# Optimization experiments

Hardware: AMD Instinct MI355X
Metric: run time of the kernel (lower is better)

Reference implementation:

```python
import jax, jax.numpy as jnp
import numpy as np

B, N = 8, 2048
IN_F, MID1, HID, MID2, OUT_F = 128, 128, 128, 128, 128
BIG = 9e15  # matches torch's 9000000000000000.0 additive mask constant


def _linear_params(key, out_d, in_d):
    # torch Linear layout: W is [out, in]
    kw, kb = jax.random.split(key)
    w = jax.random.normal(kw, (out_d, in_d), jnp.float32) * (1.0 / np.sqrt(in_d))
    b = jax.random.normal(kb, (out_d,), jnp.float32) * 0.01
    return w, b


def setup_inputs() -> dict:
    key = jax.random.key(0)
    ks = jax.random.split(key, 16)
    h = jax.random.normal(ks[0], (B, N, IN_F), jnp.float32)
    adj = jax.random.randint(ks[1], (B, N, N), 0, 2).astype(jnp.float32)
    vae2_fetures = jax.random.normal(ks[2], (B, N, OUT_F), jnp.float32)
    Wv1, bv1 = _linear_params(ks[3], MID1, IN_F)
    Wk1, bk1 = _linear_params(ks[4], MID1, IN_F)
    Wq1, bq1 = _linear_params(ks[5], MID1, IN_F)
    Wo1, bo1 = _linear_params(ks[6], HID, MID1)
    Wv2, bv2 = _linear_params(ks[7], MID2, HID)
    Wk2, bk2 = _linear_params(ks[8], MID2, HID)
    Wq2, bq2 = _linear_params(ks[9], MID2, HID)
    Wo2, bo2 = _linear_params(ks[10], OUT_F, MID2)
    Wf, bf = _linear_params(ks[11], OUT_F, 2 * OUT_F)
    return {
        "h": h, "adj": adj, "vae2_fetures": vae2_fetures,
        "Wv1": Wv1, "bv1": bv1, "Wk1": Wk1, "bk1": bk1, "Wq1": Wq1, "bq1": bq1,
        "Wo1": Wo1, "bo1": bo1,
        "Wv2": Wv2, "bv2": bv2, "Wk2": Wk2, "bk2": bk2, "Wq2": Wq2, "bq2": bq2,
        "Wo2": Wo2, "bo2": bo2, "Wf": Wf, "bf": bf,
    }


def _lin(x, W, b):
    return jnp.einsum('bnd,od->bno', x, W) + b


def _masked_att_block(x, adj, Wq, bq, Wk, bk, Wv, bv):
    v = jax.nn.relu(_lin(x, Wv, bv))          # [B,N,D]
    q = jax.nn.relu(_lin(x, Wq, bq))          # [B,N,D]
    k = jax.nn.relu(_lin(x, Wk, bk))          # [B,N,D]
    s = jnp.einsum('bnd,bmd->bnm', q, k)       # [B,N,N]
    masked = s * adj - BIG * (1.0 - adj)       # multiplicative + additive mask
    att = jax.nn.softmax(masked, axis=-1)
    return jnp.einsum('bnm,bmd->bnd', att, v)


def reference(h, adj, vae2_fetures,
              Wv1, bv1, Wk1, bk1, Wq1, bq1, Wo1, bo1,
              Wv2, bv2, Wk2, bk2, Wq2, bq2, Wo2, bo2,
              Wf, bf):
    f1 = _masked_att_block(h, adj, Wq1, bq1, Wk1, bk1, Wv1, bv1)
    f1 = _lin(f1, Wo1, bo1)                    # [B,N,HID]
    f2 = _masked_att_block(f1, adj, Wq2, bq2, Wk2, bk2, Wv2, bv2)
    f2 = _lin(f2, Wo2, bo2)                    # [B,N,OUT_F]
    f3 = jnp.concatenate([f2, vae2_fetures], axis=2)
    return _lin(f3, Wf, bf)                    # [B,N,OUT_F]
```

## Files before the change

### kernel.cpp

```cpp
#include <hip/hip_runtime.h>

typedef short s16x8 __attribute__((ext_vector_type(8)));
typedef float f32x4 __attribute__((ext_vector_type(4)));
typedef unsigned short u16x4v __attribute__((ext_vector_type(4)));

#define NEGF (-1e30f)
#define NSPLIT 4
#define NROWS 16384

__device__ __forceinline__ float bf2f(unsigned short u) {
  union { unsigned int i; float f; } v; v.i = ((unsigned int)u) << 16; return v.f;
}
__device__ __forceinline__ unsigned short f2bf(float f) {
  union { float fl; unsigned int i; } v; v.fl = f;
  unsigned int x = v.i;
  x += 0x7fffu + ((x >> 16) & 1u);
  return (unsigned short)(x >> 16);
}
__device__ __forceinline__ s16x8 load8_bf16(const unsigned short* p) {
  return *(const s16x8*)p;
}
__device__ __forceinline__ s16x8 load8_f32(const float* p) {
  float4 a = *(const float4*)p;
  float4 b = *(const float4*)(p + 4);
  s16x8 r;
  r[0] = (short)f2bf(a.x); r[1] = (short)f2bf(a.y);
  r[2] = (short)f2bf(a.z); r[3] = (short)f2bf(a.w);
  r[4] = (short)f2bf(b.x); r[5] = (short)f2bf(b.y);
  r[6] = (short)f2bf(b.z); r[7] = (short)f2bf(b.w);
  return r;
}

#define OW_Q1 0
#define OW_K1 16384
#define OW_V1 32768
#define OW_O1 49152
#define OW_Q2 65536
#define OW_K2 81920
#define OW_V2 98304
#define OW_O2 114688
#define OW_F  131072
#define OB_Q1 163840
#define OB_K1 163968
#define OB_V1 164096
#define OB_O1 164224
#define OB_Q2 164352
#define OB_K2 164480
#define OB_V2 164608
#define OB_O2 164736
#define OB_F  164864

__global__ __launch_bounds__(256) void conv_w_kernel(
    const float* s0, const float* s1, const float* s2, const float* s3,
    const float* s4, const float* s5, const float* s6, const float* s7,
    const float* s8, const float* s9, const float* s10, const float* s11,
    const float* s12, const float* s13, const float* s14, const float* s15,
    const float* s16, const float* s17, unsigned short* dst)
{
  const float* src; int count; int off;
  switch (blockIdx.y) {
    case 0:  src = s0;  count = 16384; off = OW_Q1; break;
    case 1:  src = s1;  count = 16384; off = OW_K1; break;
    case 2:  src = s2;  count = 16384; off = OW_V1; break;
    case 3:  src = s3;  count = 16384; off = OW_O1; break;
    case 4:  src = s4;  count = 16384; off = OW_Q2; break;
    case 5:  src = s5;  count = 16384; off = OW_K2; break;
    case 6:  src = s6;  count = 16384; off = OW_V2; break;
    case 7:  src = s7;  count = 16384; off = OW_O2; break;
    case 8:  src = s8;  count = 32768; off = OW_F;  break;
    case 9:  src = s9;  count = 128;   off = OB_Q1; break;
    case 10: src = s10; count = 128;   off = OB_K1; break;
    case 11: src = s11; count = 128;   off = OB_V1; break;
    case 12: src = s12; count = 128;   off = OB_O1; break;
    case 13: src = s13; count = 128;   off = OB_Q2; break;
    case 14: src = s14; count = 128;   off = OB_K2; break;
    case 15: src = s15; count = 128;   off = OB_V2; break;
    case 16: src = s16; count = 128;   off = OB_O2; break;
    default: src = s17; count = 128;   off = OB_F;  break;
  }
  for (int i = blockIdx.x * 256 + threadIdx.x; i < count; i += gridDim.x * 256)
    dst[off + i] = f2bf(src[i]);
}

__global__ __launch_bounds__(256) void pack_adj_kernel(
    const float* __restrict__ adj, unsigned long long* __restrict__ mask)
{
  const size_t stride = (size_t)gridDim.x * 256;
  const size_t total = (size_t)NROWS * 2048;
  for (size_t i = (size_t)blockIdx.x * 256 + threadIdx.x; i < total; i += stride) {
    unsigned long long m = __ballot(adj[i] != 0.0f);
    if ((threadIdx.x & 63) == 0) mask[i >> 6] = m;
  }
}

template <bool A1F32, int MODE>
__device__ __forceinline__ void gemm_body(
    const void* __restrict__ A1, const unsigned short* __restrict__ W1,
    const unsigned short* __restrict__ bias, unsigned short* __restrict__ out)
{
  const int t = threadIdx.x;
  const int w = t >> 6;
  const int lane = t & 63;
  const int l15 = lane & 15;
  const int quad = lane >> 4;
  const int mbase = blockIdx.x * 16;

  s16x8 a1[4];
  if (A1F32) {
    const float* ar = (const float*)A1 + (size_t)(mbase + l15) * 128;
#pragma unroll
    for (int ks = 0; ks < 4; ++ks) a1[ks] = load8_f32(ar + ks * 32 + quad * 8);
  } else {
    const unsigned short* ar = (const unsigned short*)A1 + (size_t)(mbase + l15) * 128;
#pragma unroll
    for (int ks = 0; ks < 4; ++ks) a1[ks] = load8_bf16(ar + ks * 32 + quad * 8);
  }

#pragma unroll
  for (int nt = 0; nt < 2; ++nt) {
    const int n = (w * 2 + nt) * 16 + l15;
    f32x4 acc = {0.f, 0.f, 0.f, 0.f};
    const unsigned short* wr = W1 + (size_t)n * 128;
#pragma unroll
    for (int ks = 0; ks < 4; ++ks)
      acc = __builtin_amdgcn_mfma_f32_16x16x32_bf16(
          a1[ks], load8_bf16(wr + ks * 32 + quad * 8), acc, 0, 0, 0);
    const float bv = bf2f(bias[n]);
    if (MODE == 0) {
#pragma unroll
      for (int r = 0; r < 4; ++r) {
        float v = fmaxf(acc[r] + bv, 0.f);
        out[(size_t)(mbase + quad * 4 + r) * 128 + n] = f2bf(v);
      }
    } else {
      const int b  = mbase >> 11;
      const int nn = (mbase & 2047) + quad * 4;
      u16x4v pk;
#pragma unroll
      for (int r = 0; r < 4; ++r) pk[r] = f2bf(fmaxf(acc[r] + bv, 0.f));
      *(u16x4v*)(out + (size_t)(b * 128 + n) * 2048 + nn) = pk;
    }
  }
}

template <bool A1F32>
__global__ __launch_bounds__(256) void qkv_kernel(
    const void* __restrict__ x,
    const unsigned short* __restrict__ Wq, const unsigned short* __restrict__ bq, unsigned short* __restrict__ oq,
    const unsigned short* __restrict__ Wk, const unsigned short* __restrict__ bk, unsigned short* __restrict__ ok,
    const unsigned short* __restrict__ Wv, const unsigned short* __restrict__ bv, unsigned short* __restrict__ ovt)
{
  if (blockIdx.y == 0)      gemm_body<A1F32, 0>(x, Wq, bq, oq);
  else if (blockIdx.y == 1) gemm_body<A1F32, 0>(x, Wk, bk, ok);
  else                      gemm_body<A1F32, 1>(x, Wv, bv, ovt);
}

__global__ __launch_bounds__(256, 2) void attn_kernel(
    const unsigned short* __restrict__ Q,
    const unsigned short* __restrict__ K,
    const unsigned short* __restrict__ VT,
    const unsigned long long* __restrict__ MASK,
    float* __restrict__ pO, float* __restrict__ pm, float* __restrict__ pl)
{
  __shared__ __align__(16) unsigned short kbuf[64][136];
  __shared__ __align__(16) unsigned short vbuf[128][72];
  __shared__ __align__(16) unsigned short pbuf[4][32][72];

  const int t = threadIdx.x;
  const int w = t >> 6;
  const int lane = t & 63;
  const int l15 = lane & 15;
  const int quad = lane >> 4;

  const int gq0 = blockIdx.x * 128;
  const int b   = gq0 >> 11;
  const int q0  = gq0 & 2047;
  const int wq0 = q0 + w * 32;
  const int kc0 = blockIdx.y * 512;
  const int kc1 = kc0 + 512;

  const unsigned short* Kb  = K  + (size_t)(b * 2048) * 128;
  const unsigned short* VTb = VT + (size_t)(b * 128) * 2048;
  const unsigned long long* Mb = MASK + (size_t)b * 2048 * 32;

  s16x8 qf[2][4];
#pragma unroll
  for (int mt = 0; mt < 2; ++mt) {
    const unsigned short* qrow = Q + (size_t)(gq0 + w * 32 + mt * 16 + l15) * 128;
#pragma unroll
    for (int ks = 0; ks < 4; ++ks) qf[mt][ks] = load8_bf16(qrow + ks * 32 + quad * 8);
  }

  float mstate[2][4], lstate[2][4];
  f32x4 accO[2][8];
#pragma unroll
  for (int mt = 0; mt < 2; ++mt) {
#pragma unroll
    for (int r = 0; r < 4; ++r) { mstate[mt][r] = NEGF; lstate[mt][r] = 0.f; }
#pragma unroll
    for (int dt = 0; dt < 8; ++dt) accO[mt][dt] = (f32x4){0.f, 0.f, 0.f, 0.f};
  }

  s16x8 kr[4], vr[4];
#pragma unroll
  for (int i = 0; i < 4; ++i) {
    int slot = i * 256 + t;
    kr[i] = load8_bf16(Kb + (size_t)(kc0 + (slot >> 4)) * 128 + (slot & 15) * 8);
    vr[i] = load8_bf16(VTb + (size_t)(slot >> 3) * 2048 + kc0 + (slot & 7) * 8);
  }

  for (int kc = kc0; kc < kc1; kc += 64) {
    __syncthreads();
#pragma unroll
    for (int i = 0; i < 4; ++i) {
      int slot = i * 256 + t;
      *(s16x8*)&kbuf[slot >> 4][(slot & 15) * 8] = kr[i];
      *(s16x8*)&vbuf[slot >> 3][(slot & 7) * 8]  = vr[i];
    }
    __syncthreads();
    if (kc + 64 < kc1) {
#pragma unroll
      for (int i = 0; i < 4; ++i) {
        int slot = i * 256 + t;
        kr[i] = load8_bf16(Kb + (size_t)(kc + 64 + (slot >> 4)) * 128 + (slot & 15) * 8);
        vr[i] = load8_bf16(VTb + (size_t)(slot >> 3) * 2048 + (kc + 64) + (slot & 7) * 8);
      }
    }

    f32x4 sv[2][4];
#pragma unroll
    for (int nt = 0; nt < 4; ++nt) {
      sv[0][nt] = (f32x4){0.f, 0.f, 0.f, 0.f};
      sv[1][nt] = (f32x4){0.f, 0.f, 0.f, 0.f};
#pragma unroll
      for (int ks = 0; ks < 4; ++ks) {
        s16x8 kf = *(const s16x8*)&kbuf[nt * 16 + l15][ks * 32 + quad * 8];
        sv[0][nt] = __builtin_amdgcn_mfma_f32_16x16x32_bf16(qf[0][ks], kf, sv[0][nt], 0, 0, 0);
        sv[1][nt] = __builtin_amdgcn_mfma_f32_16x16x32_bf16(qf[1][ks], kf, sv[1][nt], 0, 0, 0);
      }
    }

    float chmax[2][4];
#pragma unroll
    for (int mt = 0; mt < 2; ++mt) {
#pragma unroll
      for (int r = 0; r < 4; ++r) {
        unsigned long long mw = Mb[(size_t)(wq0 + mt * 16 + quad * 4 + r) * 32 + (kc >> 6)];
        float cm = NEGF;
#pragma unroll
        for (int nt = 0; nt < 4; ++nt) {
          float s = ((mw >> (nt * 16 + l15)) & 1ull) ? sv[mt][nt][r] : NEGF;
          sv[mt][nt][r] = s;
          cm = fmaxf(cm, s);
        }
        chmax[mt][r] = cm;
      }
    }
#pragma unroll
    for (int d = 1; d < 16; d <<= 1) {
#pragma unroll
      for (int mt = 0; mt < 2; ++mt)
#pragma unroll
        for (int r = 0; r < 4; ++r)
          chmax[mt][r] = fmaxf(chmax[mt][r], __shfl_xor(chmax[mt][r], d, 64));
    }

    float mnew[2][4], alpha[2][4], rsum[2][4];
#pragma unroll
    for (int mt = 0; mt < 2; ++mt)
#pragma unroll
      for (int r = 0; r < 4; ++r) {
        mnew[mt][r] = fmaxf(mstate[mt][r], chmax[mt][r]);
        alpha[mt][r] = __expf(mstate[mt][r] - mnew[mt][r]);
        rsum[mt][r] = 0.f;
      }
#pragma unroll
    for (int mt = 0; mt < 2; ++mt)
#pragma unroll
      for (int nt = 0; nt < 4; ++nt)
#pragma unroll
        for (int r = 0; r < 4; ++r) {
          float p = __expf(sv[mt][nt][r] - mnew[mt][r]);
          rsum[mt][r] += p;
          pbuf[w][mt * 16 + quad * 4 + r][nt * 16 + l15] = f2bf(p);
        }
#pragma unroll
    for (int d = 1; d < 16; d <<= 1) {
#pragma unroll
      for (int mt = 0; mt < 2; ++mt)
#pragma unroll
        for (int r = 0; r < 4; ++r)
          rsum[mt][r] += __shfl_xor(rsum[mt][r], d, 64);
    }
#pragma unroll
    for (int mt = 0; mt < 2; ++mt)
#pragma unroll
      for (int r = 0; r < 4; ++r) {
        lstate[mt][r] = lstate[mt][r] * alpha[mt][r] + rsum[mt][r];
        mstate[mt][r] = mnew[mt][r];
      }
#pragma unroll
    for (int mt = 0; mt < 2; ++mt)
#pragma unroll
      for (int dt = 0; dt < 8; ++dt)
#pragma unroll
        for (int r = 0; r < 4; ++r) accO[mt][dt][r] *= alpha[mt][r];

    s16x8 pf[2][2];
#pragma unroll
    for (int mt = 0; mt < 2; ++mt)
#pragma unroll
      for (int ks = 0; ks < 2; ++ks)
        pf[mt][ks] = *(const s16x8*)&pbuf[w][mt * 16 + l15][ks * 32 + quad * 8];
#pragma unroll
    for (int dt = 0; dt < 8; ++dt) {
#pragma unroll
      for (int ks = 0; ks < 2; ++ks) {
        s16x8 vf = *(const s16x8*)&vbuf[dt * 16 + l15][ks * 32 + quad * 8];
        accO[0][dt] = __builtin_amdgcn_mfma_f32_16x16x32_bf16(pf[0][ks], vf, accO[0][dt], 0, 0, 0);
        accO[1][dt] = __builtin_amdgcn_mfma_f32_16x16x32_bf16(pf[1][ks], vf, accO[1][dt], 0, 0, 0);
      }
    }
  }

  float* pOs = pO + (size_t)blockIdx.y * NROWS * 128;
#pragma unroll
  for (int mt = 0; mt < 2; ++mt)
#pragma unroll
    for (int dt = 0; dt < 8; ++dt) {
      int dcol = dt * 16 + l15;
#pragma unroll
      for (int r = 0; r < 4; ++r) {
        int qg = gq0 + w * 32 + mt * 16 + quad * 4 + r;
        pOs[(size_t)qg * 128 + dcol] = accO[mt][dt][r];
      }
    }
  if (l15 == 0) {
#pragma unroll
    for (int mt = 0; mt < 2; ++mt)
#pragma unroll
      for (int r = 0; r < 4; ++r) {
        int qg = gq0 + w * 32 + mt * 16 + quad * 4 + r;
        pm[blockIdx.y * NROWS + qg] = mstate[mt][r];
        pl[blockIdx.y * NROWS + qg] = lstate[mt][r];
      }
  }
}

template <bool FINAL>
__global__ __launch_bounds__(256) void red_lin_kernel(
    const float* __restrict__ pO, const float* __restrict__ pm,
    const float* __restrict__ pl,
    const unsigned short* __restrict__ Wo, const unsigned short* __restrict__ bo,
    const unsigned short* __restrict__ Wf, const float* __restrict__ vae2,
    const unsigned short* __restrict__ bfb,
    unsigned short* __restrict__ out_bf, float* __restrict__ out_f32)
{
  __shared__ __align__(16) unsigned short At[16][136];
  __shared__ __align__(16) unsigned short Bt[16][136];

  const int t = threadIdx.x;
  const int grow0 = blockIdx.x * 16;

  {
    const int row = t >> 4;
    const int col8 = (t & 15) * 8;
    const int grow = grow0 + row;
    float ms[NSPLIT], mstar = NEGF;
#pragma unroll
    for (int s = 0; s < NSPLIT; ++s) {
      ms[s] = pm[s * NROWS + grow];
      mstar = fmaxf(mstar, ms[s]);
    }
    float wgt[NSPLIT], lstar = 0.f;
#pragma unroll
    for (int s = 0; s < NSPLIT; ++s) {
      wgt[s] = __expf(ms[s] - mstar);
      lstar += wgt[s] * pl[s * NROWS + grow];
    }
    const float inv = (lstar > 0.f) ? 1.f / lstar : 0.f;
    float acc8[8];
#pragma unroll
    for (int i = 0; i < 8; ++i) acc8[i] = 0.f;
#pragma unroll
    for (int s = 0; s < NSPLIT; ++s) {
      const float* p = pO + (size_t)s * NROWS * 128 + (size_t)grow * 128 + col8;
      float4 x0 = *(const float4*)p;
      float4 x1 = *(const float4*)(p + 4);
      acc8[0] += wgt[s] * x0.x; acc8[1] += wgt[s] * x0.y;
      acc8[2] += wgt[s] * x0.z; acc8[3] += wgt[s] * x0.w;
      acc8[4] += wgt[s] * x1.x; acc8[5] += wgt[s] * x1.y;
      acc8[6] += wgt[s] * x1.z; acc8[7] += wgt[s] * x1.w;
    }
#pragma unroll
    for (int i = 0; i < 8; ++i) At[row][col8 + i] = f2bf(acc8[i] * inv);
  }
  __syncthreads();

  const int w = t >> 6;
  const int lane = t & 63;
  const int l15 = lane & 15;
  const int quad = lane >> 4;

  s16x8 a[4];
#pragma unroll
  for (int ks = 0; ks < 4; ++ks) a[ks] = *(const s16x8*)&At[l15][ks * 32 + quad * 8];
#pragma unroll
  for (int nt = 0; nt < 2; ++nt) {
    const int n = (w * 2 + nt) * 16 + l15;
    f32x4 acc = {0.f, 0.f, 0.f, 0.f};
    const unsigned short* wr = Wo + (size_t)n * 128;
#pragma unroll
    for (int ks = 0; ks < 4; ++ks)
      acc = __builtin_amdgcn_mfma_f32_16x16x32_bf16(
          a[ks], load8_bf16(wr + ks * 32 + quad * 8), acc, 0, 0, 0);
    const float bv = bf2f(bo[n]);
    if (!FINAL) {
#pragma unroll
      for (int r = 0; r < 4; ++r)
        out_bf[(size_t)(grow0 + quad * 4 + r) * 128 + n] = f2bf(acc[r] + bv);
    } else {
#pragma unroll
      for (int r = 0; r < 4; ++r)
        Bt[quad * 4 + r][n] = f2bf(acc[r] + bv);
    }
  }

  if (FINAL) {
    __syncthreads();
    s16x8 a1[4], a2[4];
#pragma unroll
    for (int ks = 0; ks < 4; ++ks) a1[ks] = *(const s16x8*)&Bt[l15][ks * 32 + quad * 8];
    const float* vrow = vae2 + (size_t)(grow0 + l15) * 128;
#pragma unroll
    for (int ks = 0; ks < 4; ++ks) a2[ks] = load8_f32(vrow + ks * 32 + quad * 8);
#pragma unroll
    for (int nt = 0; nt < 2; ++nt) {
      const int n = (w * 2 + nt) * 16 + l15;
      f32x4 acc = {0.f, 0.f, 0.f, 0.f};
      const unsigned short* wr = Wf + (size_t)n * 256;
#pragma unroll
      for (int ks = 0; ks < 4; ++ks)
        acc = __builtin_amdgcn_mfma_f32_16x16x32_bf16(
            a1[ks], load8_bf16(wr + ks * 32 + quad * 8), acc, 0, 0, 0);
#pragma unroll
      for (int ks = 0; ks < 4; ++ks)
        acc = __builtin_amdgcn_mfma_f32_16x16x32_bf16(
            a2[ks], load8_bf16(wr + 128 + ks * 32 + quad * 8), acc, 0, 0, 0);
      const float bv = bf2f(bfb[n]);
#pragma unroll
      for (int r = 0; r < 4; ++r)
        out_f32[(size_t)(grow0 + quad * 4 + r) * 128 + n] = acc[r] + bv;
    }
  }
}

extern "C" void kernel_launch(void* const* d_in, const int* in_sizes, int n_in,
                              void* d_out, int out_size, void* d_ws, size_t ws_size,
                              hipStream_t stream)
{
  const float* h    = (const float*)d_in[0];
  const float* adj  = (const float*)d_in[1];
  const float* vae2 = (const float*)d_in[2];
  const float* Wv1  = (const float*)d_in[3];
  const float* bv1  = (const float*)d_in[4];
  const float* Wk1  = (const float*)d_in[5];
  const float* bk1  = (const float*)d_in[6];
  const float* Wq1  = (const float*)d_in[7];
  const float* bq1  = (const float*)d_in[8];
  const float* Wo1  = (const float*)d_in[9];
  const float* bo1  = (const float*)d_in[10];
  const float* Wv2  = (const float*)d_in[11];
  const float* bv2  = (const float*)d_in[12];
  const float* Wk2  = (const float*)d_in[13];
  const float* bk2  = (const float*)d_in[14];
  const float* Wq2  = (const float*)d_in[15];
  const float* bq2  = (const float*)d_in[16];
  const float* Wo2  = (const float*)d_in[17];
  const float* bo2  = (const float*)d_in[18];
  const float* Wf   = (const float*)d_in[19];
  const float* bff  = (const float*)d_in[20];

  char* wsb = (char*)d_ws;
  const size_t MB = 1u << 20;
  unsigned short* s_q  = (unsigned short*)(wsb + 0 * MB);
  unsigned short* s_k  = (unsigned short*)(wsb + 4 * MB);
  unsigned short* s_vt = (unsigned short*)(wsb + 8 * MB);
  unsigned short* s_f  = (unsigned short*)(wsb + 12 * MB);
  unsigned short* wbf  = (unsigned short*)(wsb + 16 * MB);
  unsigned long long* maskp = (unsigned long long*)(wsb + 17 * MB);
  float* pO = (float*)(wsb + 21 * MB);
  float* pm = (float*)(wsb + 53 * MB);
  float* pl = (float*)(wsb + 53 * MB + 512 * 1024);

  dim3 blk(256);
  conv_w_kernel<<<dim3(128, 18), blk, 0, stream>>>(
      Wq1, Wk1, Wv1, Wo1, Wq2, Wk2, Wv2, Wo2, Wf,
      bq1, bk1, bv1, bo1, bq2, bk2, bv2, bo2, bff, wbf);
  pack_adj_kernel<<<dim3(8192), blk, 0, stream>>>(adj, maskp);

  qkv_kernel<true><<<dim3(1024, 3), blk, 0, stream>>>(
      h, wbf + OW_Q1, wbf + OB_Q1, s_q,
         wbf + OW_K1, wbf + OB_K1, s_k,
         wbf + OW_V1, wbf + OB_V1, s_vt);
  attn_kernel<<<dim3(128, NSPLIT), blk, 0, stream>>>(s_q, s_k, s_vt, maskp, pO, pm, pl);
  red_lin_kernel<false><<<dim3(1024), blk, 0, stream>>>(
      pO, pm, pl, wbf + OW_O1, wbf + OB_O1, nullptr, nullptr, nullptr, s_f, nullptr);

  qkv_kernel<false><<<dim3(1024, 3), blk, 0, stream>>>(
      s_f, wbf + OW_Q2, wbf + OB_Q2, s_q,
           wbf + OW_K2, wbf + OB_K2, s_k,
           wbf + OW_V2, wbf + OB_V2, s_vt);
  attn_kernel<<<dim3(128, NSPLIT), blk, 0, stream>>>(s_q, s_k, s_vt, maskp, pO, pm, pl);
  red_lin_kernel<true><<<dim3(1024), blk, 0, stream>>>(
      pO, pm, pl, wbf + OW_O2, wbf + OB_O2, wbf + OW_F, vae2, wbf + OB_F,
      nullptr, (float*)d_out);
}
```

Before: 429.0 us.

## Fuse reduce with next QKV, drop weight conversion, reshape attention without LDS staging

The standalone weight-conversion kernel is removed, and the GEMMs now read fp32 weights directly, converting them to bf16 on the fly. The split-combine plus output-projection kernel is fused with the second layer's QKV projection, which removes one launch and the round trip of the intermediate features. The attention kernel moves to 128-thread blocks over 64 query rows and reads K and V fragments straight from global memory instead of double-buffering them in LDS. The adjacency packer now uses float4 loads and shuffle-OR reductions. The risks are more redundant global and L2 traffic for K/V and weights, and repeated fp32-to-bf16 conversion in every block.

```diff
diff --git a/kernel.cpp b/kernel.cpp
--- a/kernel.cpp
+++ b/kernel.cpp
@@ -8,9 +8,6 @@
 #define NSPLIT 4
 #define NROWS 16384
 
-__device__ __forceinline__ float bf2f(unsigned short u) {
-  union { unsigned int i; float f; } v; v.i = ((unsigned int)u) << 16; return v.f;
-}
 __device__ __forceinline__ unsigned short f2bf(float f) {
   union { float fl; unsigned int i; } v; v.fl = f;
   unsigned int x = v.i;
@@ -31,72 +28,29 @@
   return r;
 }
 
-#define OW_Q1 0
-#define OW_K1 16384
-#define OW_V1 32768
-#define OW_O1 49152
-#define OW_Q2 65536
-#define OW_K2 81920
-#define OW_V2 98304
-#define OW_O2 114688
-#define OW_F  131072
-#define OB_Q1 163840
-#define OB_K1 163968
-#define OB_V1 164096
-#define OB_O1 164224
-#define OB_Q2 164352
-#define OB_K2 164480
-#define OB_V2 164608
-#define OB_O2 164736
-#define OB_F  164864
-
-__global__ __launch_bounds__(256) void conv_w_kernel(
-    const float* s0, const float* s1, const float* s2, const float* s3,
-    const float* s4, const float* s5, const float* s6, const float* s7,
-    const float* s8, const float* s9, const float* s10, const float* s11,
-    const float* s12, const float* s13, const float* s14, const float* s15,
-    const float* s16, const float* s17, unsigned short* dst)
-{
-  const float* src; int count; int off;
-  switch (blockIdx.y) {
-    case 0:  src = s0;  count = 16384; off = OW_Q1; break;
-    case 1:  src = s1;  count = 16384; off = OW_K1; break;
-    case 2:  src = s2;  count = 16384; off = OW_V1; break;
-    case 3:  src = s3;  count = 16384; off = OW_O1; break;
-    case 4:  src = s4;  count = 16384; off = OW_Q2; break;
-    case 5:  src = s5;  count = 16384; off = OW_K2; break;
-    case 6:  src = s6;  count = 16384; off = OW_V2; break;
-    case 7:  src = s7;  count = 16384; off = OW_O2; break;
-    case 8:  src = s8;  count = 32768; off = OW_F;  break;
-    case 9:  src = s9;  count = 128;   off = OB_Q1; break;
-    case 10: src = s10; count = 128;   off = OB_K1; break;
-    case 11: src = s11; count = 128;   off = OB_V1; break;
-    case 12: src = s12; count = 128;   off = OB_O1; break;
-    case 13: src = s13; count = 128;   off = OB_Q2; break;
-    case 14: src = s14; count = 128;   off = OB_K2; break;
-    case 15: src = s15; count = 128;   off = OB_V2; break;
-    case 16: src = s16; count = 128;   off = OB_O2; break;
-    default: src = s17; count = 128;   off = OB_F;  break;
-  }
-  for (int i = blockIdx.x * 256 + threadIdx.x; i < count; i += gridDim.x * 256)
-    dst[off + i] = f2bf(src[i]);
-}
-
-__global__ __launch_bounds__(256) void pack_adj_kernel(
-    const float* __restrict__ adj, unsigned long long* __restrict__ mask)
-{
+__global__ __launch_bounds__(256) void pack_kernel(
+    const float4* __restrict__ adj4, unsigned long long* __restrict__ mask)
+{
+  const int lane = threadIdx.x & 63;
+  const size_t nvec = (size_t)NROWS * 2048 / 4;
   const size_t stride = (size_t)gridDim.x * 256;
-  const size_t total = (size_t)NROWS * 2048;
-  for (size_t i = (size_t)blockIdx.x * 256 + threadIdx.x; i < total; i += stride) {
-    unsigned long long m = __ballot(adj[i] != 0.0f);
-    if ((threadIdx.x & 63) == 0) mask[i >> 6] = m;
-  }
-}
-
-template <bool A1F32, int MODE>
-__device__ __forceinline__ void gemm_body(
-    const void* __restrict__ A1, const unsigned short* __restrict__ W1,
-    const unsigned short* __restrict__ bias, unsigned short* __restrict__ out)
+  for (size_t i = (size_t)blockIdx.x * 256 + threadIdx.x; i < nvec; i += stride) {
+    float4 v = adj4[i];
+    unsigned long long n = (v.x != 0.f ? 1u : 0u) | (v.y != 0.f ? 2u : 0u) |
+                           (v.z != 0.f ? 4u : 0u) | (v.w != 0.f ? 8u : 0u);
+    unsigned long long word = n << (4 * (lane & 15));
+    word |= __shfl_xor(word, 1, 64);
+    word |= __shfl_xor(word, 2, 64);
+    word |= __shfl_xor(word, 4, 64);
+    word |= __shfl_xor(word, 8, 64);
+    if ((lane & 15) == 0) mask[(i * 4) >> 6] = word;
+  }
+}
+
+template <int MODE>
+__device__ __forceinline__ void qkv_body(
+    const float* __restrict__ X, const float* __restrict__ W,
+    const float* __restrict__ bias, unsigned short* __restrict__ out)
 {
   const int t = threadIdx.x;
   const int w = t >> 6;
@@ -105,33 +59,25 @@
   const int quad = lane >> 4;
   const int mbase = blockIdx.x * 16;
 
-  s16x8 a1[4];
-  if (A1F32) {
-    const float* ar = (const float*)A1 + (size_t)(mbase + l15) * 128;
-#pragma unroll
-    for (int ks = 0; ks < 4; ++ks) a1[ks] = load8_f32(ar + ks * 32 + quad * 8);
-  } else {
-    const unsigned short* ar = (const unsigned short*)A1 + (size_t)(mbase + l15) * 128;
-#pragma unroll
-    for (int ks = 0; ks < 4; ++ks) a1[ks] = load8_bf16(ar + ks * 32 + quad * 8);
-  }
+  s16x8 a[4];
+  const float* ar = X + (size_t)(mbase + l15) * 128;
+#pragma unroll
+  for (int ks = 0; ks < 4; ++ks) a[ks] = load8_f32(ar + ks * 32 + quad * 8);
 
 #pragma unroll
   for (int nt = 0; nt < 2; ++nt) {
     const int n = (w * 2 + nt) * 16 + l15;
     f32x4 acc = {0.f, 0.f, 0.f, 0.f};
-    const unsigned short* wr = W1 + (size_t)n * 128;
+    const float* wr = W + (size_t)n * 128;
 #pragma unroll
     for (int ks = 0; ks < 4; ++ks)
       acc = __builtin_amdgcn_mfma_f32_16x16x32_bf16(
-          a1[ks], load8_bf16(wr + ks * 32 + quad * 8), acc, 0, 0, 0);
-    const float bv = bf2f(bias[n]);
+          a[ks], load8_f32(wr + ks * 32 + quad * 8), acc, 0, 0, 0);
+    const float bv = bias[n];
     if (MODE == 0) {
 #pragma unroll
-      for (int r = 0; r < 4; ++r) {
-        float v = fmaxf(acc[r] + bv, 0.f);
-        out[(size_t)(mbase + quad * 4 + r) * 128 + n] = f2bf(v);
-      }
+      for (int r = 0; r < 4; ++r)
+        out[(size_t)(mbase + quad * 4 + r) * 128 + n] = f2bf(fmaxf(acc[r] + bv, 0.f));
     } else {
       const int b  = mbase >> 11;
       const int nn = (mbase & 2047) + quad * 4;
@@ -143,28 +89,25 @@
   }
 }
 
-template <bool A1F32>
-__global__ __launch_bounds__(256) void qkv_kernel(
-    const void* __restrict__ x,
-    const unsigned short* __restrict__ Wq, const unsigned short* __restrict__ bq, unsigned short* __restrict__ oq,
-    const unsigned short* __restrict__ Wk, const unsigned short* __restrict__ bk, unsigned short* __restrict__ ok,
-    const unsigned short* __restrict__ Wv, const unsigned short* __restrict__ bv, unsigned short* __restrict__ ovt)
-{
-  if (blockIdx.y == 0)      gemm_body<A1F32, 0>(x, Wq, bq, oq);
-  else if (blockIdx.y == 1) gemm_body<A1F32, 0>(x, Wk, bk, ok);
-  else                      gemm_body<A1F32, 1>(x, Wv, bv, ovt);
-}
-
-__global__ __launch_bounds__(256, 2) void attn_kernel(
+__global__ __launch_bounds__(256) void qkv1_kernel(
+    const float* __restrict__ x,
+    const float* __restrict__ Wq, const float* __restrict__ bq, unsigned short* __restrict__ oq,
+    const float* __restrict__ Wk, const float* __restrict__ bk, unsigned short* __restrict__ ok,
+    const float* __restrict__ Wv, const float* __restrict__ bv, unsigned short* __restrict__ ovt)
+{
+  if (blockIdx.y == 0)      qkv_body<0>(x, Wq, bq, oq);
+  else if (blockIdx.y == 1) qkv_body<0>(x, Wk, bk, ok);
+  else                      qkv_body<1>(x, Wv, bv, ovt);
+}
+
+__global__ __launch_bounds__(128, 2) void attn_kernel(
     const unsigned short* __restrict__ Q,
     const unsigned short* __restrict__ K,
     const unsigned short* __restrict__ VT,
     const unsigned long long* __restrict__ MASK,
     float* __restrict__ pO, float* __restrict__ pm, float* __restrict__ pl)
 {
-  __shared__ __align__(16) unsigned short kbuf[64][136];
-  __shared__ __align__(16) unsigned short vbuf[128][72];
-  __shared__ __align__(16) unsigned short pbuf[4][32][72];
+  __shared__ __align__(16) unsigned short pbuf[2][32][72];
 
   const int t = threadIdx.x;
   const int w = t >> 6;
@@ -172,12 +115,11 @@
   const int l15 = lane & 15;
   const int quad = lane >> 4;
 
-  const int gq0 = blockIdx.x * 128;
+  const int gq0 = blockIdx.x * 64;
   const int b   = gq0 >> 11;
   const int q0  = gq0 & 2047;
   const int wq0 = q0 + w * 32;
   const int kc0 = blockIdx.y * 512;
-  const int kc1 = kc0 + 512;
 
   const unsigned short* Kb  = K  + (size_t)(b * 2048) * 128;
   const unsigned short* VTb = VT + (size_t)(b * 128) * 2048;
@@ -201,40 +143,16 @@
     for (int dt = 0; dt < 8; ++dt) accO[mt][dt] = (f32x4){0.f, 0.f, 0.f, 0.f};
   }
 
-  s16x8 kr[4], vr[4];
-#pragma unroll
-  for (int i = 0; i < 4; ++i) {
-    int slot = i * 256 + t;
-    kr[i] = load8_bf16(Kb + (size_t)(kc0 + (slot >> 4)) * 128 + (slot & 15) * 8);
-    vr[i] = load8_bf16(VTb + (size_t)(slot >> 3) * 2048 + kc0 + (slot & 7) * 8);
-  }
-
-  for (int kc = kc0; kc < kc1; kc += 64) {
-    __syncthreads();
-#pragma unroll
-    for (int i = 0; i < 4; ++i) {
-      int slot = i * 256 + t;
-      *(s16x8*)&kbuf[slot >> 4][(slot & 15) * 8] = kr[i];
-      *(s16x8*)&vbuf[slot >> 3][(slot & 7) * 8]  = vr[i];
-    }
-    __syncthreads();
-    if (kc + 64 < kc1) {
-#pragma unroll
-      for (int i = 0; i < 4; ++i) {
-        int slot = i * 256 + t;
-        kr[i] = load8_bf16(Kb + (size_t)(kc + 64 + (slot >> 4)) * 128 + (slot & 15) * 8);
-        vr[i] = load8_bf16(VTb + (size_t)(slot >> 3) * 2048 + (kc + 64) + (slot & 7) * 8);
-      }
-    }
-
+  for (int kc = kc0; kc < kc0 + 512; kc += 64) {
     f32x4 sv[2][4];
 #pragma unroll
     for (int nt = 0; nt < 4; ++nt) {
       sv[0][nt] = (f32x4){0.f, 0.f, 0.f, 0.f};
       sv[1][nt] = (f32x4){0.f, 0.f, 0.f, 0.f};
+      const unsigned short* krow = Kb + (size_t)(kc + nt * 16 + l15) * 128;
 #pragma unroll
       for (int ks = 0; ks < 4; ++ks) {
-        s16x8 kf = *(const s16x8*)&kbuf[nt * 16 + l15][ks * 32 + quad * 8];
+        s16x8 kf = load8_bf16(krow + ks * 32 + quad * 8);
         sv[0][nt] = __builtin_amdgcn_mfma_f32_16x16x32_bf16(qf[0][ks], kf, sv[0][nt], 0, 0, 0);
         sv[1][nt] = __builtin_amdgcn_mfma_f32_16x16x32_bf16(qf[1][ks], kf, sv[1][nt], 0, 0, 0);
       }
@@ -257,13 +175,12 @@
       }
     }
 #pragma unroll
-    for (int d = 1; d < 16; d <<= 1) {
+    for (int d = 1; d < 16; d <<= 1)
 #pragma unroll
       for (int mt = 0; mt < 2; ++mt)
 #pragma unroll
         for (int r = 0; r < 4; ++r)
           chmax[mt][r] = fmaxf(chmax[mt][r], __shfl_xor(chmax[mt][r], d, 64));
-    }
 
     float mnew[2][4], alpha[2][4], rsum[2][4];
 #pragma unroll
@@ -285,13 +202,12 @@
           pbuf[w][mt * 16 + quad * 4 + r][nt * 16 + l15] = f2bf(p);
         }
 #pragma unroll
-    for (int d = 1; d < 16; d <<= 1) {
+    for (int d = 1; d < 16; d <<= 1)
 #pragma unroll
       for (int mt = 0; mt < 2; ++mt)
 #pragma unroll
         for (int r = 0; r < 4; ++r)
           rsum[mt][r] += __shfl_xor(rsum[mt][r], d, 64);
-    }
 #pragma unroll
     for (int mt = 0; mt < 2; ++mt)
 #pragma unroll
@@ -312,11 +228,13 @@
 #pragma unroll
       for (int ks = 0; ks < 2; ++ks)
         pf[mt][ks] = *(const s16x8*)&pbuf[w][mt * 16 + l15][ks * 32 + quad * 8];
+
 #pragma unroll
     for (int dt = 0; dt < 8; ++dt) {
+      const unsigned short* vrow = VTb + (size_t)(dt * 16 + l15) * 2048 + kc;
 #pragma unroll
       for (int ks = 0; ks < 2; ++ks) {
-        s16x8 vf = *(const s16x8*)&vbuf[dt * 16 + l15][ks * 32 + quad * 8];
+        s16x8 vf = load8_bf16(vrow + ks * 32 + quad * 8);
         accO[0][dt] = __builtin_amdgcn_mfma_f32_16x16x32_bf16(pf[0][ks], vf, accO[0][dt], 0, 0, 0);
         accO[1][dt] = __builtin_amdgcn_mfma_f32_16x16x32_bf16(pf[1][ks], vf, accO[1][dt], 0, 0, 0);
       }
@@ -347,54 +265,58 @@
   }
 }
 
-template <bool FINAL>
-__global__ __launch_bounds__(256) void red_lin_kernel(
+__device__ __forceinline__ void combine_splits(
     const float* __restrict__ pO, const float* __restrict__ pm,
-    const float* __restrict__ pl,
-    const unsigned short* __restrict__ Wo, const unsigned short* __restrict__ bo,
-    const unsigned short* __restrict__ Wf, const float* __restrict__ vae2,
-    const unsigned short* __restrict__ bfb,
-    unsigned short* __restrict__ out_bf, float* __restrict__ out_f32)
+    const float* __restrict__ pl, int grow0,
+    unsigned short (*At)[136])
+{
+  const int t = threadIdx.x;
+  const int row = t >> 4;
+  const int col8 = (t & 15) * 8;
+  const int grow = grow0 + row;
+  float ms[NSPLIT], mstar = NEGF;
+#pragma unroll
+  for (int s = 0; s < NSPLIT; ++s) {
+    ms[s] = pm[s * NROWS + grow];
+    mstar = fmaxf(mstar, ms[s]);
+  }
+  float wgt[NSPLIT], lstar = 0.f;
+#pragma unroll
+  for (int s = 0; s < NSPLIT; ++s) {
+    wgt[s] = __expf(ms[s] - mstar);
+    lstar += wgt[s] * pl[s * NROWS + grow];
+  }
+  const float inv = (lstar > 0.f) ? 1.f / lstar : 0.f;
+  float acc8[8];
+#pragma unroll
+  for (int i = 0; i < 8; ++i) acc8[i] = 0.f;
+#pragma unroll
+  for (int s = 0; s < NSPLIT; ++s) {
+    const float* p = pO + (size_t)s * NROWS * 128 + (size_t)grow * 128 + col8;
+    float4 x0 = *(const float4*)p;
+    float4 x1 = *(const float4*)(p + 4);
+    acc8[0] += wgt[s] * x0.x; acc8[1] += wgt[s] * x0.y;
+    acc8[2] += wgt[s] * x0.z; acc8[3] += wgt[s] * x0.w;
+    acc8[4] += wgt[s] * x1.x; acc8[5] += wgt[s] * x1.y;
+    acc8[6] += wgt[s] * x1.z; acc8[7] += wgt[s] * x1.w;
+  }
+#pragma unroll
+  for (int i = 0; i < 8; ++i) At[row][col8 + i] = f2bf(acc8[i] * inv);
+}
+
+__global__ __launch_bounds__(256) void redqkv_kernel(
+    const float* __restrict__ pO, const float* __restrict__ pm, const float* __restrict__ pl,
+    const float* __restrict__ Wo, const float* __restrict__ bo,
+    const float* __restrict__ Wq, const float* __restrict__ bq, unsigned short* __restrict__ oq,
+    const float* __restrict__ Wk, const float* __restrict__ bk, unsigned short* __restrict__ ok,
+    const float* __restrict__ Wv, const float* __restrict__ bv, unsigned short* __restrict__ ovt)
 {
   __shared__ __align__(16) unsigned short At[16][136];
   __shared__ __align__(16) unsigned short Bt[16][136];
-
   const int t = threadIdx.x;
   const int grow0 = blockIdx.x * 16;
 
-  {
-    const int row = t >> 4;
-    const int col8 = (t & 15) * 8;
-    const int grow = grow0 + row;
-    float ms[NSPLIT], mstar = NEGF;
-#pragma unroll
-    for (int s = 0; s < NSPLIT; ++s) {
-      ms[s] = pm[s * NROWS + grow];
-      mstar = fmaxf(mstar, ms[s]);
-    }
-    float wgt[NSPLIT], lstar = 0.f;
-#pragma unroll
-    for (int s = 0; s < NSPLIT; ++s) {
-      wgt[s] = __expf(ms[s] - mstar);
-      lstar += wgt[s] * pl[s * NROWS + grow];
-    }
-    const float inv = (lstar > 0.f) ? 1.f / lstar : 0.f;
-    float acc8[8];
-#pragma unroll
-    for (int i = 0; i < 8; ++i) acc8[i] = 0.f;
-#pragma unroll
-    for (int s = 0; s < NSPLIT; ++s) {
-      const float* p = pO + (size_t)s * NROWS * 128 + (size_t)grow * 128 + col8;
-      float4 x0 = *(const float4*)p;
-      float4 x1 = *(const float4*)(p + 4);
-      acc8[0] += wgt[s] * x0.x; acc8[1] += wgt[s] * x0.y;
-      acc8[2] += wgt[s] * x0.z; acc8[3] += wgt[s] * x0.w;
-      acc8[4] += wgt[s] * x1.x; acc8[5] += wgt[s] * x1.y;
-      acc8[6] += wgt[s] * x1.z; acc8[7] += wgt[s] * x1.w;
-    }
-#pragma unroll
-    for (int i = 0; i < 8; ++i) At[row][col8 + i] = f2bf(acc8[i] * inv);
-  }
+  combine_splits(pO, pm, pl, grow0, At);
   __syncthreads();
 
   const int w = t >> 6;
@@ -409,49 +331,112 @@
   for (int nt = 0; nt < 2; ++nt) {
     const int n = (w * 2 + nt) * 16 + l15;
     f32x4 acc = {0.f, 0.f, 0.f, 0.f};
-    const unsigned short* wr = Wo + (size_t)n * 128;
+    const float* wr = Wo + (size_t)n * 128;
 #pragma unroll
     for (int ks = 0; ks < 4; ++ks)
       acc = __builtin_amdgcn_mfma_f32_16x16x32_bf16(
-          a[ks], load8_bf16(wr + ks * 32 + quad * 8), acc, 0, 0, 0);
-    const float bv = bf2f(bo[n]);
-    if (!FINAL) {
-#pragma unroll
-      for (int r = 0; r < 4; ++r)
-        out_bf[(size_t)(grow0 + quad * 4 + r) * 128 + n] = f2bf(acc[r] + bv);
-    } else {
-#pragma unroll
-      for (int r = 0; r < 4; ++r)
-        Bt[quad * 4 + r][n] = f2bf(acc[r] + bv);
-    }
-  }
-
-  if (FINAL) {
-    __syncthreads();
-    s16x8 a1[4], a2[4];
-#pragma unroll
-    for (int ks = 0; ks < 4; ++ks) a1[ks] = *(const s16x8*)&Bt[l15][ks * 32 + quad * 8];
-    const float* vrow = vae2 + (size_t)(grow0 + l15) * 128;
-#pragma unroll
-    for (int ks = 0; ks < 4; ++ks) a2[ks] = load8_f32(vrow + ks * 32 + quad * 8);
+          a[ks], load8_f32(wr + ks * 32 + quad * 8), acc, 0, 0, 0);
+    const float bv_ = bo[n];
+#pragma unroll
+    for (int r = 0; r < 4; ++r) Bt[quad * 4 + r][n] = f2bf(acc[r] + bv_);
+  }
+  __syncthreads();
+
+  s16x8 a2[4];
+#pragma unroll
+  for (int ks = 0; ks < 4; ++ks) a2[ks] = *(const s16x8*)&Bt[l15][ks * 32 + quad * 8];
+
+#pragma unroll
+  for (int which = 0; which < 3; ++which) {
+    const float* W = (which == 0) ? Wq : (which == 1) ? Wk : Wv;
+    const float* bb = (which == 0) ? bq : (which == 1) ? bk : bv;
+    unsigned short* out = (which == 0) ? oq : (which == 1) ? ok : ovt;
 #pragma unroll
     for (int nt = 0; nt < 2; ++nt) {
       const int n = (w * 2 + nt) * 16 + l15;
       f32x4 acc = {0.f, 0.f, 0.f, 0.f};
-      const unsigned short* wr = Wf + (size_t)n * 256;
+      const float* wr = W + (size_t)n * 128;
 #pragma unroll
       for (int ks = 0; ks < 4; ++ks)
         acc = __builtin_amdgcn_mfma_f32_16x16x32_bf16(
-            a1[ks], load8_bf16(wr + ks * 32 + quad * 8), acc, 0, 0, 0);
-#pragma unroll
-      for (int ks = 0; ks < 4; ++ks)
-        acc = __builtin_amdgcn_mfma_f32_16x16x32_bf16(
-            a2[ks], load8_bf16(wr + 128 + ks * 32 + quad * 8), acc, 0, 0, 0);
-      const float bv = bf2f(bfb[n]);
-#pragma unroll
-      for (int r = 0; r < 4; ++r)
-        out_f32[(size_t)(grow0 + quad * 4 + r) * 128 + n] = acc[r] + bv;
-    }
+            a2[ks], load8_f32(wr + ks * 32 + quad * 8), acc, 0, 0, 0);
+      const float bv_ = bb[n];
+      if (which < 2) {
+#pragma unroll
+        for (int r = 0; r < 4; ++r)
+          out[(size_t)(grow0 + quad * 4 + r) * 128 + n] = f2bf(fmaxf(acc[r] + bv_, 0.f));
+      } else {
+        const int b  = grow0 >> 11;
+        const int nn = (grow0 & 2047) + quad * 4;
+        u16x4v pk;
+#pragma unroll
+        for (int r = 0; r < 4; ++r) pk[r] = f2bf(fmaxf(acc[r] + bv_, 0.f));
+        *(u16x4v*)(out + (size_t)(b * 128 + n) * 2048 + nn) = pk;
+      }
+    }
+  }
+}
+
+__global__ __launch_bounds__(256) void redfinal_kernel(
+    const float* __restrict__ pO, const float* __restrict__ pm, const float* __restrict__ pl,
+    const float* __restrict__ Wo, const float* __restrict__ bo,
+    const float* __restrict__ Wf, const float* __restrict__ bff,
+    const float* __restrict__ vae2, float* __restrict__ out)
+{
+  __shared__ __align__(16) unsigned short At[16][136];
+  __shared__ __align__(16) unsigned short Bt[16][136];
+  const int t = threadIdx.x;
+  const int grow0 = blockIdx.x * 16;
+
+  combine_splits(pO, pm, pl, grow0, At);
+  __syncthreads();
+
+  const int w = t >> 6;
+  const int lane = t & 63;
+  const int l15 = lane & 15;
+  const int quad = lane >> 4;
+
+  s16x8 a[4];
+#pragma unroll
+  for (int ks = 0; ks < 4; ++ks) a[ks] = *(const s16x8*)&At[l15][ks * 32 + quad * 8];
+#pragma unroll
+  for (int nt = 0; nt < 2; ++nt) {
+    const int n = (w * 2 + nt) * 16 + l15;
+    f32x4 acc = {0.f, 0.f, 0.f, 0.f};
+    const float* wr = Wo + (size_t)n * 128;
+#pragma unroll
+    for (int ks = 0; ks < 4; ++ks)
+      acc = __builtin_amdgcn_mfma_f32_16x16x32_bf16(
+          a[ks], load8_f32(wr + ks * 32 + quad * 8), acc, 0, 0, 0);
+    const float bv_ = bo[n];
+#pragma unroll
+    for (int r = 0; r < 4; ++r) Bt[quad * 4 + r][n] = f2bf(acc[r] + bv_);
+  }
+  __syncthreads();
+
+  s16x8 a1[4], a2[4];
+#pragma unroll
+  for (int ks = 0; ks < 4; ++ks) a1[ks] = *(const s16x8*)&Bt[l15][ks * 32 + quad * 8];
+  const float* vrow = vae2 + (size_t)(grow0 + l15) * 128;
+#pragma unroll
+  for (int ks = 0; ks < 4; ++ks) a2[ks] = load8_f32(vrow + ks * 32 + quad * 8);
+#pragma unroll
+  for (int nt = 0; nt < 2; ++nt) {
+    const int n = (w * 2 + nt) * 16 + l15;
+    f32x4 acc = {0.f, 0.f, 0.f, 0.f};
+    const float* wr = Wf + (size_t)n * 256;
+#pragma unroll
+    for (int ks = 0; ks < 4; ++ks)
+      acc = __builtin_amdgcn_mfma_f32_16x16x32_bf16(
+          a1[ks], load8_f32(wr + ks * 32 + quad * 8), acc, 0, 0, 0);
+#pragma unroll
+    for (int ks = 0; ks < 4; ++ks)
+      acc = __builtin_amdgcn_mfma_f32_16x16x32_bf16(
+          a2[ks], load8_f32(wr + 128 + ks * 32 + quad * 8), acc, 0, 0, 0);
+    const float bv_ = bff[n];
+#pragma unroll
+    for (int r = 0; r < 4; ++r)
+      out[(size_t)(grow0 + quad * 4 + r) * 128 + n] = acc[r] + bv_;
   }
 }
 
@@ -486,33 +471,20 @@
   unsigned short* s_q  = (unsigned short*)(wsb + 0 * MB);
   unsigned short* s_k  = (unsigned short*)(wsb + 4 * MB);
   unsigned short* s_vt = (unsigned short*)(wsb + 8 * MB);
-  unsigned short* s_f  = (unsigned short*)(wsb + 12 * MB);
-  unsigned short* wbf  = (unsigned short*)(wsb + 16 * MB);
-  unsigned long long* maskp = (unsigned long long*)(wsb + 17 * MB);
-  float* pO = (float*)(wsb + 21 * MB);
-  float* pm = (float*)(wsb + 53 * MB);
-  float* pl = (float*)(wsb + 53 * MB + 512 * 1024);
-
-  dim3 blk(256);
-  conv_w_kernel<<<dim3(128, 18), blk, 0, stream>>>(
-      Wq1, Wk1, Wv1, Wo1, Wq2, Wk2, Wv2, Wo2, Wf,
-      bq1, bk1, bv1, bo1, bq2, bk2, bv2, bo2, bff, wbf);
-  pack_adj_kernel<<<dim3(8192), blk, 0, stream>>>(adj, maskp);
-
-  qkv_kernel<true><<<dim3(1024, 3), blk, 0, stream>>>(
-      h, wbf + OW_Q1, wbf + OB_Q1, s_q,
-         wbf + OW_K1, wbf + OB_K1, s_k,
-         wbf + OW_V1, wbf + OB_V1, s_vt);
-  attn_kernel<<<dim3(128, NSPLIT), blk, 0, stream>>>(s_q, s_k, s_vt, maskp, pO, pm, pl);
-  red_lin_kernel<false><<<dim3(1024), blk, 0, stream>>>(
-      pO, pm, pl, wbf + OW_O1, wbf + OB_O1, nullptr, nullptr, nullptr, s_f, nullptr);
-
-  qkv_kernel<false><<<dim3(1024, 3), blk, 0, stream>>>(
-      s_f, wbf + OW_Q2, wbf + OB_Q2, s_q,
-           wbf + OW_K2, wbf + OB_K2, s_k,
-           wbf + OW_V2, wbf + OB_V2, s_vt);
-  attn_kernel<<<dim3(128, NSPLIT), blk, 0, stream>>>(s_q, s_k, s_vt, maskp, pO, pm, pl);
-  red_lin_kernel<true><<<dim3(1024), blk, 0, stream>>>(
-      pO, pm, pl, wbf + OW_O2, wbf + OB_O2, wbf + OW_F, vae2, wbf + OB_F,
-      nullptr, (float*)d_out);
-}
+  unsigned long long* maskp = (unsigned long long*)(wsb + 12 * MB);
+  float* pO = (float*)(wsb + 16 * MB);
+  float* pm = (float*)(wsb + 48 * MB);
+  float* pl = (float*)(wsb + 48 * MB + 512 * 1024);
+
+  pack_kernel<<<dim3(4096), dim3(256), 0, stream>>>((const float4*)adj, maskp);
+  qkv1_kernel<<<dim3(1024, 3), dim3(256), 0, stream>>>(
+      h, Wq1, bq1, s_q, Wk1, bk1, s_k, Wv1, bv1, s_vt);
+  attn_kernel<<<dim3(256, NSPLIT), dim3(128), 0, stream>>>(
+      s_q, s_k, s_vt, maskp, pO, pm, pl);
+  redqkv_kernel<<<dim3(1024), dim3(256), 0, stream>>>(
+      pO, pm, pl, Wo1, bo1, Wq2, bq2, s_q, Wk2, bk2, s_k, Wv2, bv2, s_vt);
+  attn_kernel<<<dim3(256, NSPLIT), dim3(128), 0, stream>>>(
+      s_q, s_k, s_vt, maskp, pO, pm, pl);
+  redfinal_kernel<<<dim3(1024), dim3(256), 0, stream>>>(
+      pO, pm, pl, Wo2, bo2, Wf, bff, vae2, (float*)d_out);
+}
```

Result: slower. 481.7 us (+12.3%).
